# Kernel tuning notes

Hardware: AMD Instinct MI355X
Metric: run time of the kernel (lower is better)

The kernel has to match this reference:

```python
import jax, jax.numpy as jnp
import numpy as np

HIDDEN = 128
N_RBF = 20
K = 16
CUTOFF = 5.0


def setup_inputs() -> dict:
    key = jax.random.key(0)
    ks = jax.random.split(key, 12)
    B, N, D = 8, 4096, HIDDEN
    edge_in = 2 * D + N_RBF  # 276
    s = 0.02
    return {
        "h": jax.random.normal(ks[0], (B, N, D), jnp.float32),
        "positions": jax.random.normal(ks[1], (B, N, 3), jnp.float32),
        # edge MLP: Linear(276->128), SiLU, Linear(128->128), SiLU
        "ew1": jax.random.normal(ks[2], (edge_in, D), jnp.float32) * s,
        "eb1": jnp.zeros((D,), jnp.float32),
        "ew2": jax.random.normal(ks[3], (D, D), jnp.float32) * s,
        "eb2": jnp.zeros((D,), jnp.float32),
        # node MLP: Linear(256->128), SiLU, (Dropout=identity in eval), Linear(128->128)
        "nw1": jax.random.normal(ks[4], (2 * D, D), jnp.float32) * s,
        "nb1": jnp.zeros((D,), jnp.float32),
        "nw2": jax.random.normal(ks[5], (D, D), jnp.float32) * s,
        "nb2": jnp.zeros((D,), jnp.float32),
        # LayerNorm
        "gamma": jnp.ones((D,), jnp.float32),
        "beta": jnp.zeros((D,), jnp.float32),
    }


def reference(h, positions, ew1, eb1, ew2, eb2, nw1, nb1, nw2, nb2, gamma, beta):
    B, N, D = h.shape
    k = min(K, N - 1)

    # ---- kNN graph build (dense pairwise, self masked with +inf) ----
    diff = positions[:, :, None, :] - positions[:, None, :, :]      # [B,N,N,3]
    dists = jnp.sqrt(jnp.sum(diff * diff, axis=-1) + 1e-8)          # [B,N,N]
    eye = jnp.eye(N, dtype=bool)
    dists_masked = jnp.where(eye[None], jnp.inf, dists)
    _, edge_idx = jax.lax.top_k(-dists_masked, k)                   # [B,N,k] smallest dists
    edge_dist = jnp.take_along_axis(dists_masked, edge_idx, axis=-1)  # [B,N,k]
    edge_mask = edge_dist < CUTOFF                                  # [B,N,k]

    # ---- RBF distance encoding (non-trainable buffers) ----
    centers = jnp.linspace(0.0, CUTOFF, N_RBF)                      # [n_rbf]
    widths = (CUTOFF / N_RBF) ** (-2)
    rbf = jnp.exp(-widths * (edge_dist[..., None] - centers) ** 2)  # [B,N,k,n_rbf]

    # ---- gather neighbor features ----
    h_j = jax.vmap(lambda hb, ib: hb[ib])(h, edge_idx)              # [B,N,k,D]
    h_i = jnp.broadcast_to(h[:, :, None, :], h_j.shape)             # [B,N,k,D]
    edge_features = jnp.concatenate([h_i, h_j, rbf], axis=-1)       # [B,N,k,2D+n_rbf]

    # ---- edge MLP + mask + scatter-sum aggregate ----
    m = jax.nn.silu(edge_features @ ew1 + eb1)
    m = jax.nn.silu(m @ ew2 + eb2)
    m = m * edge_mask[..., None].astype(m.dtype)
    agg = jnp.sum(m, axis=2)                                        # [B,N,D]

    # ---- node MLP (dropout is identity at eval) + residual + LayerNorm ----
    node_in = jnp.concatenate([h, agg], axis=-1)                    # [B,N,2D]
    update = jax.nn.silu(node_in @ nw1 + nb1) @ nw2 + nb2
    x = h + update
    mu = jnp.mean(x, axis=-1, keepdims=True)
    var = jnp.mean((x - mu) ** 2, axis=-1, keepdims=True)
    return (x - mu) / jnp.sqrt(var + 1e-5) * gamma + beta
```

## Files before the change

kernel.cpp:

```cpp
#include <hip/hip_runtime.h>

#define HID 128
#define NRBF 20
#define KNN 16
#define NNODE 4096
#define NBATCH 8
#define CAP 112

typedef __attribute__((ext_vector_type(8))) short short8;
typedef __attribute__((ext_vector_type(4))) float f32x4;

__device__ __forceinline__ short f2bf(float x) {
  unsigned u = __builtin_bit_cast(unsigned, x);
  u = u + 0x7FFFu + ((u >> 16) & 1u);
  return (short)(u >> 16);
}
__device__ __forceinline__ float silu_f(float x) {
  return x * __builtin_amdgcn_rcpf(1.0f + __expf(-x));
}
__device__ __forceinline__ short8 cv8(const float* p) {
  f32x4 a = *(const f32x4*)p;
  f32x4 b = *(const f32x4*)(p + 4);
  short8 r;
  r[0]=f2bf(a[0]); r[1]=f2bf(a[1]); r[2]=f2bf(a[2]); r[3]=f2bf(a[3]);
  r[4]=f2bf(b[0]); r[5]=f2bf(b[1]); r[6]=f2bf(b[2]); r[7]=f2bf(b[3]);
  return r;
}

__global__ __launch_bounds__(256)
void hcvt_kernel(const float* __restrict__ h, short* __restrict__ hb)
{
  size_t i = ((size_t)blockIdx.x * 256 + threadIdx.x) * 8;
  *(short8*)(hb + i) = cv8(h + i);
}

__global__ __launch_bounds__(512)
void knn_kernel(const float* __restrict__ pos,
                int* __restrict__ eidx, float* __restrict__ edist)
{
  __shared__ float pX[NNODE], pY[NNODE], pZ[NNODE];
  __shared__ float d2b[8][4][CAP];
  __shared__ int   jb[8][4][CAP];
  __shared__ int   cntL[8][4];

  const int tid  = threadIdx.x;
  const int wv   = tid >> 6;
  const int lane = tid & 63;
  const int b    = blockIdx.x >> 7;
  const int grp  = blockIdx.x & 127;

  const float* pb = pos + (size_t)b * NNODE * 3;
  for (int idx = tid; idx < NNODE; idx += 512) {
    pX[idx] = pb[idx*3]; pY[idx] = pb[idx*3+1]; pZ[idx] = pb[idx*3+2];
  }
  __syncthreads();

  const int i0 = grp * 32 + wv * 4;
  float pix[4], piy[4], piz[4];
  #pragma unroll
  for (int n = 0; n < 4; ++n) { pix[n]=pX[i0+n]; piy[n]=pY[i0+n]; piz[n]=pZ[i0+n]; }

  float vmin0[4] = {3.0e38f, 3.0e38f, 3.0e38f, 3.0e38f};
  float vmin1[4] = {3.0e38f, 3.0e38f, 3.0e38f, 3.0e38f};
  #pragma unroll 4
  for (int t = 0; t < 64; t += 2) {
    const int j0 = t*64 + lane, j1 = j0 + 64;
    const float x0 = pX[j0], y0 = pY[j0], z0 = pZ[j0];
    const float x1 = pX[j1], y1 = pY[j1], z1 = pZ[j1];
    #pragma unroll
    for (int n = 0; n < 4; ++n) {
      float dx0 = pix[n]-x0, dy0 = piy[n]-y0, dz0 = piz[n]-z0;
      vmin0[n] = fminf(vmin0[n], fmaf(dz0,dz0, fmaf(dy0,dy0, dx0*dx0)));
      float dx1 = pix[n]-x1, dy1 = piy[n]-y1, dz1 = piz[n]-z1;
      vmin1[n] = fminf(vmin1[n], fmaf(dz1,dz1, fmaf(dy1,dy1, dx1*dx1)));
    }
  }

  float Tp[4];
  #pragma unroll
  for (int n = 0; n < 4; ++n) {
    float v = fminf(vmin0[n], vmin1[n]);
    #pragma unroll
    for (int k = 2; k <= 64; k <<= 1) {
      #pragma unroll
      for (int jj = k >> 1; jj > 0; jj >>= 1) {
        float o = __shfl_xor(v, jj);
        const bool up   = ((lane & k) == 0);
        const bool lowl = ((lane & jj) == 0);
        float mn = fminf(v, o), mx = fmaxf(v, o);
        v = (up == lowl) ? mn : mx;
      }
    }
    float Tf = __shfl(v, 16);
    Tp[n] = Tf * (1.0f + 2.0e-6f) + 1.0e-35f;
  }

  if (lane < 4) cntL[wv][lane] = 0;
  #pragma unroll 2
  for (int t = 0; t < 64; ++t) {
    const int j = t * 64 + lane;
    const float x = pX[j], y = pY[j], z = pZ[j];
    #pragma unroll
    for (int n = 0; n < 4; ++n) {
      float dx = pix[n] - x, dy = piy[n] - y, dz = piz[n] - z;
      float d2 = fmaf(dz, dz, fmaf(dy, dy, dx * dx));
      if ((j != i0 + n) && (d2 <= Tp[n])) {
        int p = atomicAdd(&cntL[wv][n], 1);
        if (p < CAP) jb[wv][n][p] = j;
      }
    }
  }

  #pragma unroll 1
  for (int n = 0; n < 4; ++n) {
    int cnt = cntL[wv][n];
    if (cnt > CAP) cnt = CAP;
    for (int s = lane; s < cnt; s += 64) {
      int j = jb[wv][n][s];
      float dx = __fsub_rn(pix[n], pX[j]);
      float dy = __fsub_rn(piy[n], pY[j]);
      float dz = __fsub_rn(piz[n], pZ[j]);
      d2b[wv][n][s] = __fadd_rn(__fadd_rn(__fmul_rn(dx,dx), __fmul_rn(dy,dy)),
                                __fmul_rn(dz,dz));
    }
    for (int s = lane; s < cnt; s += 64) {
      float dm = d2b[wv][n][s]; int jm = jb[wv][n][s];
      int rank = 0;
      for (int c = 0; c < cnt; ++c) {
        float dc = d2b[wv][n][c]; int jc = jb[wv][n][c];
        if (dc < dm || (dc == dm && jc < jm)) ++rank;
      }
      if (rank < KNN) {
        size_t base = ((size_t)b * NNODE + i0 + n) * KNN;
        eidx[base + rank]  = b * NNODE + jm;
        edist[base + rank] = sqrtf(__fadd_rn(dm, 1e-8f));
      }
    }
  }
}

#define ENPW 16

template<bool HBF>
__global__ __launch_bounds__(512)
void edge_kernel(const float* __restrict__ h, const short* __restrict__ hb,
                 const int* __restrict__ eidx, const float* __restrict__ edist,
                 const float* __restrict__ ew1, const float* __restrict__ eb1,
                 const float* __restrict__ ew2, const float* __restrict__ eb2,
                 float* __restrict__ agg)
{
  __shared__ __attribute__((aligned(16))) short8 F1[9*8*64];
  __shared__ __attribute__((aligned(16))) short8 F2[4*8*64];
  __shared__ __attribute__((aligned(16))) short m1s[8][2048];

  const int tid = threadIdx.x;
  for (int f = tid; f < 9*8*64; f += 512) {
    int kc = f >> 9, rem = f & 511, nf = rem >> 6, ln = rem & 63;
    int kb = kc*32 + (ln >> 4)*8, col = nf*16 + (ln & 15);
    short8 v;
    #pragma unroll
    for (int e = 0; e < 8; ++e) {
      int k = kb + e;
      v[e] = (k < 276) ? f2bf(ew1[k*128 + col]) : (short)0;
    }
    F1[f] = v;
  }
  for (int f = tid; f < 4*8*64; f += 512) {
    int kc = f >> 9, rem = f & 511, nf = rem >> 6, ln = rem & 63;
    int kb = kc*32 + (ln >> 4)*8, col = nf*16 + (ln & 15);
    short8 v;
    #pragma unroll
    for (int e = 0; e < 8; ++e) v[e] = f2bf(ew2[(kb + e)*128 + col]);
    F2[f] = v;
  }
  __syncthreads();

  const int wv = tid >> 6, lane = tid & 63;
  const int lo = lane & 15, hi = lane >> 4;
  short* m1w = &m1s[wv][0];

  float b1v[8], b2v[8];
  #pragma unroll
  for (int nf = 0; nf < 8; ++nf) {
    b1v[nf] = eb1[nf*16 + lo];
    b2v[nf] = eb2[nf*16 + lo];
  }
  int wbase[4], xmask[4], rbase[4];
  #pragma unroll
  for (int q = 0; q < 4; ++q) {
    int row = hi*4 + q;
    wbase[q] = (row << 8) + (lo << 1);
    xmask[q] = (row & 7) << 4;
  }
  #pragma unroll
  for (int kc = 0; kc < 4; ++kc)
    rbase[kc] = ((lo << 8) + ((kc*32 + hi*8) << 1)) ^ ((lo & 7) << 4);

  const f32x4 zero4 = {0.f, 0.f, 0.f, 0.f};
  const int swz = (blockIdx.x & 7) * 32 + (blockIdx.x >> 3);
  const int nbase = (swz * 8 + wv) * ENPW;

  #pragma unroll 1
  for (int it = 0; it < ENPW/2; ++it) {
    const int nA = nbase + it*2, nB = nA + 1;
    int jgA = eidx[(size_t)nA*KNN + lo] & (NBATCH*NNODE - 1);
    int jgB = eidx[(size_t)nB*KNN + lo] & (NBATCH*NNODE - 1);
    const float deA = edist[(size_t)nA*KNN + lo];
    const float deB = edist[(size_t)nB*KNN + lo];

    short8 aIA[4], aJA[4], aIB[4], aJB[4];
    #pragma unroll
    for (int kc = 0; kc < 4; ++kc) {
      if constexpr (HBF) {
        aIA[kc] = *(const short8*)(hb + (size_t)nA*HID  + kc*32 + hi*8);
        aJA[kc] = *(const short8*)(hb + (size_t)jgA*HID + kc*32 + hi*8);
        aIB[kc] = *(const short8*)(hb + (size_t)nB*HID  + kc*32 + hi*8);
        aJB[kc] = *(const short8*)(hb + (size_t)jgB*HID + kc*32 + hi*8);
      } else {
        aIA[kc] = cv8(h + (size_t)nA*HID  + kc*32 + hi*8);
        aJA[kc] = cv8(h + (size_t)jgA*HID + kc*32 + hi*8);
        aIB[kc] = cv8(h + (size_t)nB*HID  + kc*32 + hi*8);
        aJB[kc] = cv8(h + (size_t)jgB*HID + kc*32 + hi*8);
      }
    }
    short8 aRA, aRB;
    #pragma unroll
    for (int e = 0; e < 8; ++e) {
      const int r = hi*8 + e;
      float vA = 0.f, vB = 0.f;
      if (r < NRBF) {
        const float cr = (float)(r * (5.0/19.0));
        float tA = __fsub_rn(deA, cr), tB = __fsub_rn(deB, cr);
        vA = __expf(-16.0f * __fmul_rn(tA, tA));
        vB = __expf(-16.0f * __fmul_rn(tB, tB));
      }
      aRA[e] = f2bf(vA); aRB[e] = f2bf(vB);
    }

    f32x4 acc1A[8], acc1B[8];
    #pragma unroll
    for (int nf = 0; nf < 8; ++nf) { acc1A[nf] = zero4; acc1B[nf] = zero4; }
    __builtin_amdgcn_s_setprio(1);
    #pragma unroll
    for (int kc = 0; kc < 9; ++kc) {
      short8 aA = (kc < 4) ? aIA[kc] : ((kc < 8) ? aJA[kc-4] : aRA);
      short8 aB = (kc < 4) ? aIB[kc] : ((kc < 8) ? aJB[kc-4] : aRB);
      #pragma unroll
      for (int nf = 0; nf < 8; ++nf) {
        short8 bfv = F1[(kc*8 + nf)*64 + lane];
        acc1A[nf] = __builtin_amdgcn_mfma_f32_16x16x32_bf16(aA, bfv, acc1A[nf], 0,0,0);
        acc1B[nf] = __builtin_amdgcn_mfma_f32_16x16x32_bf16(aB, bfv, acc1B[nf], 0,0,0);
      }
    }
    __builtin_amdgcn_s_setprio(0);

    short8 a2A[4], a2B[4];
    #pragma unroll
    for (int nf = 0; nf < 8; ++nf) {
      #pragma unroll
      for (int q = 0; q < 4; ++q) {
        int off = (wbase[q] + (nf << 5)) ^ xmask[q];
        *(short*)((char*)m1w + off) = f2bf(silu_f(acc1A[nf][q] + b1v[nf]));
      }
    }
    #pragma unroll
    for (int kc = 0; kc < 4; ++kc)
      a2A[kc] = *(const short8*)((char*)m1w + rbase[kc]);
    #pragma unroll
    for (int nf = 0; nf < 8; ++nf) {
      #pragma unroll
      for (int q = 0; q < 4; ++q) {
        int off = (wbase[q] + (nf << 5)) ^ xmask[q];
        *(short*)((char*)m1w + off) = f2bf(silu_f(acc1B[nf][q] + b1v[nf]));
      }
    }
    #pragma unroll
    for (int kc = 0; kc < 4; ++kc)
      a2B[kc] = *(const short8*)((char*)m1w + rbase[kc]);

    f32x4 acc2A[8], acc2B[8];
    #pragma unroll
    for (int nf = 0; nf < 8; ++nf) { acc2A[nf] = zero4; acc2B[nf] = zero4; }
    __builtin_amdgcn_s_setprio(1);
    #pragma unroll
    for (int kc = 0; kc < 4; ++kc) {
      #pragma unroll
      for (int nf = 0; nf < 8; ++nf) {
        short8 bfv = F2[(kc*8 + nf)*64 + lane];
        acc2A[nf] = __builtin_amdgcn_mfma_f32_16x16x32_bf16(a2A[kc], bfv, acc2A[nf], 0,0,0);
        acc2B[nf] = __builtin_amdgcn_mfma_f32_16x16x32_bf16(a2B[kc], bfv, acc2B[nf], 0,0,0);
      }
    }
    __builtin_amdgcn_s_setprio(0);

    float dqA[4], dqB[4];
    #pragma unroll
    for (int q = 0; q < 4; ++q) {
      dqA[q] = __shfl(deA, hi*4 + q);
      dqB[q] = __shfl(deB, hi*4 + q);
    }
    #pragma unroll
    for (int nf = 0; nf < 8; ++nf) {
      float sA = 0.f, sB = 0.f;
      #pragma unroll
      for (int q = 0; q < 4; ++q) {
        float mA = silu_f(acc2A[nf][q] + b2v[nf]);
        float mB = silu_f(acc2B[nf][q] + b2v[nf]);
        sA += (dqA[q] < 5.0f) ? mA : 0.f;
        sB += (dqB[q] < 5.0f) ? mB : 0.f;
      }
      sA += __shfl_xor(sA, 16); sA += __shfl_xor(sA, 32);
      sB += __shfl_xor(sB, 16); sB += __shfl_xor(sB, 32);
      if (hi == 0) {
        agg[(size_t)nA*HID + nf*16 + lo] = sA;
        agg[(size_t)nB*HID + nf*16 + lo] = sB;
      }
    }
  }
}

template<bool HBF>
__global__ __launch_bounds__(512)
void node_kernel(const float* __restrict__ h, const short* __restrict__ hb,
                 const float* agg,
                 const float* __restrict__ nw1, const float* __restrict__ nb1,
                 const float* __restrict__ nw2, const float* __restrict__ nb2,
                 const float* __restrict__ gam, const float* __restrict__ bet,
                 float* out)
{
  __shared__ __attribute__((aligned(16))) short8 G1[8*8*64];
  __shared__ __attribute__((aligned(16))) short8 G2[4*8*64];
  __shared__ __attribute__((aligned(16))) short m1s[8][2048];

  const int tid = threadIdx.x;
  for (int f = tid; f < 8*8*64; f += 512) {
    int kc = f >> 9, rem = f & 511, nf = rem >> 6, ln = rem & 63;
    int kb = kc*32 + (ln >> 4)*8, col = nf*16 + (ln & 15);
    short8 v;
    #pragma unroll
    for (int e = 0; e < 8; ++e) v[e] = f2bf(nw1[(kb + e)*128 + col]);
    G1[f] = v;
  }
  for (int f = tid; f < 4*8*64; f += 512) {
    int kc = f >> 9, rem = f & 511, nf = rem >> 6, ln = rem & 63;
    int kb = kc*32 + (ln >> 4)*8, col = nf*16 + (ln & 15);
    short8 v;
    #pragma unroll
    for (int e = 0; e < 8; ++e) v[e] = f2bf(nw2[(kb + e)*128 + col]);
    G2[f] = v;
  }
  __syncthreads();

  const int wv = tid >> 6, lane = tid & 63;
  const int lo = lane & 15, hi = lane >> 4;
  short* m1w = &m1s[wv][0];

  float b1v[8], b2v[8], gv[8], bv[8];
  #pragma unroll
  for (int nf = 0; nf < 8; ++nf) {
    b1v[nf] = nb1[nf*16 + lo];
    b2v[nf] = nb2[nf*16 + lo];
    gv[nf]  = gam[nf*16 + lo];
    bv[nf]  = bet[nf*16 + lo];
  }
  const f32x4 zero4 = {0.f, 0.f, 0.f, 0.f};

  const int row0 = (blockIdx.x * 8 + wv) * 16;

  const float* hrow = h   + (size_t)(row0 + lo) * HID;
  const float* arow = agg + (size_t)(row0 + lo) * HID;
  const short* hbrow = hb + (size_t)(row0 + lo) * HID;

  f32x4 acc1[8];
  #pragma unroll
  for (int nf = 0; nf < 8; ++nf) acc1[nf] = zero4;
  #pragma unroll
  for (int kc = 0; kc < 8; ++kc) {
    short8 a;
    if (kc < 4) {
      if constexpr (HBF) a = *(const short8*)(hbrow + kc*32 + hi*8);
      else               a = cv8(hrow + kc*32 + hi*8);
    } else {
      a = cv8(arow + (kc - 4)*32 + hi*8);
    }
    #pragma unroll
    for (int nf = 0; nf < 8; ++nf) {
      short8 bfv = G1[(kc*8 + nf)*64 + lane];
      acc1[nf] = __builtin_amdgcn_mfma_f32_16x16x32_bf16(a, bfv, acc1[nf], 0,0,0);
    }
  }

  #pragma unroll
  for (int nf = 0; nf < 8; ++nf) {
    #pragma unroll
    for (int q = 0; q < 4; ++q) {
      float s = silu_f(acc1[nf][q] + b1v[nf]);
      int row = hi*4 + q, col = nf*16 + lo;
      int byteoff = ((row << 8) + (col << 1)) ^ ((row & 7) << 4);
      *(short*)((char*)m1w + byteoff) = f2bf(s);
    }
  }

  f32x4 acc2[8];
  #pragma unroll
  for (int nf = 0; nf < 8; ++nf) acc2[nf] = zero4;
  #pragma unroll
  for (int kc = 0; kc < 4; ++kc) {
    int byteA = ((lo << 8) + ((kc*32 + hi*8) << 1)) ^ ((lo & 7) << 4);
    short8 a = *(const short8*)((char*)m1w + byteA);
    #pragma unroll
    for (int nf = 0; nf < 8; ++nf) {
      short8 bfv = G2[(kc*8 + nf)*64 + lane];
      acc2[nf] = __builtin_amdgcn_mfma_f32_16x16x32_bf16(a, bfv, acc2[nf], 0,0,0);
    }
  }

  float xv[4][8];
  #pragma unroll
  for (int nf = 0; nf < 8; ++nf) {
    #pragma unroll
    for (int q = 0; q < 4; ++q) {
      xv[q][nf] = acc2[nf][q] + b2v[nf]
                + h[(size_t)(row0 + hi*4 + q) * HID + nf*16 + lo];
    }
  }

  #pragma unroll
  for (int q = 0; q < 4; ++q) {
    float s = 0.0f;
    #pragma unroll
    for (int nf = 0; nf < 8; ++nf) s += xv[q][nf];
    s += __shfl_xor(s, 1); s += __shfl_xor(s, 2);
    s += __shfl_xor(s, 4); s += __shfl_xor(s, 8);
    float mu = s * 0.0078125f;
    float t = 0.0f;
    #pragma unroll
    for (int nf = 0; nf < 8; ++nf) { float d = xv[q][nf] - mu; t += d * d; }
    t += __shfl_xor(t, 1); t += __shfl_xor(t, 2);
    t += __shfl_xor(t, 4); t += __shfl_xor(t, 8);
    float inv = 1.0f / sqrtf(t * 0.0078125f + 1e-5f);
    #pragma unroll
    for (int nf = 0; nf < 8; ++nf) {
      float y = (xv[q][nf] - mu) * inv * gv[nf] + bv[nf];
      out[(size_t)(row0 + hi*4 + q) * HID + nf*16 + lo] = y;
    }
  }
}

extern "C" void kernel_launch(void* const* d_in, const int* in_sizes, int n_in,
                              void* d_out, int out_size, void* d_ws, size_t ws_size,
                              hipStream_t stream) {
  (void)in_sizes; (void)n_in; (void)out_size;
  const float* h   = (const float*)d_in[0];
  const float* pos = (const float*)d_in[1];
  const float* ew1 = (const float*)d_in[2];
  const float* eb1 = (const float*)d_in[3];
  const float* ew2 = (const float*)d_in[4];
  const float* eb2 = (const float*)d_in[5];
  const float* nw1 = (const float*)d_in[6];
  const float* nb1 = (const float*)d_in[7];
  const float* nw2 = (const float*)d_in[8];
  const float* nb2 = (const float*)d_in[9];
  const float* gam = (const float*)d_in[10];
  const float* bet = (const float*)d_in[11];

  const size_t base_need = (size_t)NBATCH * NNODE * KNN * 8;
  const size_t hbf_need  = base_need + (size_t)NBATCH * NNODE * HID * 2;
  if (ws_size < base_need) return;
  const bool use_hbf = (ws_size >= hbf_need);

  char* wsp = (char*)d_ws;
  int*   eidx  = (int*)wsp;
  float* edist = (float*)(wsp + (size_t)NBATCH * NNODE * KNN * 4);
  short* hb    = (short*)(wsp + base_need);
  float* agg   = (float*)d_out;

  if (use_hbf) {
    hcvt_kernel<<<dim3(2048), dim3(256), 0, stream>>>(h, hb);
  }
  knn_kernel<<<dim3(1024), dim3(512), 0, stream>>>(pos, eidx, edist);
  if (use_hbf) {
    edge_kernel<true ><<<dim3(256), dim3(512), 0, stream>>>(h, hb, eidx, edist,
                                                            ew1, eb1, ew2, eb2, agg);
    node_kernel<true ><<<dim3(256), dim3(512), 0, stream>>>(h, hb, agg, nw1, nb1,
                                                            nw2, nb2, gam, bet, (float*)d_out);
  } else {
    edge_kernel<false><<<dim3(256), dim3(512), 0, stream>>>(h, hb, eidx, edist,
                                                            ew1, eb1, ew2, eb2, agg);
    node_kernel<false><<<dim3(256), dim3(512), 0, stream>>>(h, hb, agg, nw1, nb1,
                                                            nw2, nb2, gam, bet, (float*)d_out);
  }
}
```

Measured before the change: 204.1 us.

## Use packed fp16 kNN prefilter and split edge MLP into two kernels

The kNN kernel now stores positions in shared memory as packed half2 and runs the threshold and candidate-filter passes in fp16. The threshold is widened to absorb fp16 error, and exact distances are recomputed in fp32 from global memory. The fused edge kernel is split into edge1 and edge2 kernels that pass a bf16 hidden activation through a large workspace buffer. This aims to cut kNN ALU and LDS cost and raise edge-MLP occupancy, at the price of extra global traffic. A looser threshold can overflow the candidate capacity, and fp16 may misrank near-ties.

```diff
diff --git a/kernel.cpp b/kernel.cpp
--- a/kernel.cpp
+++ b/kernel.cpp
@@ -9,6 +9,7 @@
 
 typedef __attribute__((ext_vector_type(8))) short short8;
 typedef __attribute__((ext_vector_type(4))) float f32x4;
+typedef __attribute__((ext_vector_type(2))) _Float16 h2;
 
 __device__ __forceinline__ short f2bf(float x) {
   unsigned u = __builtin_bit_cast(unsigned, x);
@@ -38,7 +39,7 @@
 void knn_kernel(const float* __restrict__ pos,
                 int* __restrict__ eidx, float* __restrict__ edist)
 {
-  __shared__ float pX[NNODE], pY[NNODE], pZ[NNODE];
+  __shared__ h2 pHx[NNODE/2], pHy[NNODE/2], pHz[NNODE/2];
   __shared__ float d2b[8][4][CAP];
   __shared__ int   jb[8][4][CAP];
   __shared__ int   cntL[8][4];
@@ -50,36 +51,49 @@
   const int grp  = blockIdx.x & 127;
 
   const float* pb = pos + (size_t)b * NNODE * 3;
-  for (int idx = tid; idx < NNODE; idx += 512) {
-    pX[idx] = pb[idx*3]; pY[idx] = pb[idx*3+1]; pZ[idx] = pb[idx*3+2];
+  for (int k = tid; k < NNODE/2; k += 512) {
+    h2 vx, vy, vz;
+    vx[0] = (_Float16)pb[(2*k)*3];   vx[1] = (_Float16)pb[(2*k+1)*3];
+    vy[0] = (_Float16)pb[(2*k)*3+1]; vy[1] = (_Float16)pb[(2*k+1)*3+1];
+    vz[0] = (_Float16)pb[(2*k)*3+2]; vz[1] = (_Float16)pb[(2*k+1)*3+2];
+    pHx[k] = vx; pHy[k] = vy; pHz[k] = vz;
   }
   __syncthreads();
 
   const int i0 = grp * 32 + wv * 4;
-  float pix[4], piy[4], piz[4];
-  #pragma unroll
-  for (int n = 0; n < 4; ++n) { pix[n]=pX[i0+n]; piy[n]=pY[i0+n]; piz[n]=pZ[i0+n]; }
-
-  float vmin0[4] = {3.0e38f, 3.0e38f, 3.0e38f, 3.0e38f};
-  float vmin1[4] = {3.0e38f, 3.0e38f, 3.0e38f, 3.0e38f};
-  #pragma unroll 4
-  for (int t = 0; t < 64; t += 2) {
-    const int j0 = t*64 + lane, j1 = j0 + 64;
-    const float x0 = pX[j0], y0 = pY[j0], z0 = pZ[j0];
-    const float x1 = pX[j1], y1 = pY[j1], z1 = pZ[j1];
+  float pixf[4], piyf[4], pizf[4];
+  h2 px2[4], py2[4], pz2[4];
+  #pragma unroll
+  for (int n = 0; n < 4; ++n) {
+    pixf[n] = pb[(i0+n)*3]; piyf[n] = pb[(i0+n)*3+1]; pizf[n] = pb[(i0+n)*3+2];
+    _Float16 hx = (_Float16)pixf[n], hy = (_Float16)piyf[n], hz = (_Float16)pizf[n];
+    px2[n][0] = hx; px2[n][1] = hx;
+    py2[n][0] = hy; py2[n][1] = hy;
+    pz2[n][0] = hz; pz2[n][1] = hz;
+  }
+
+  h2 vmin2[4];
+  #pragma unroll
+  for (int n = 0; n < 4; ++n) { vmin2[n][0] = (_Float16)6.0e4f; vmin2[n][1] = (_Float16)6.0e4f; }
+  #pragma unroll 2
+  for (int t = 0; t < 32; ++t) {
+    const int k = t*64 + lane;
+    h2 xh = pHx[k], yh = pHy[k], zh = pHz[k];
     #pragma unroll
     for (int n = 0; n < 4; ++n) {
-      float dx0 = pix[n]-x0, dy0 = piy[n]-y0, dz0 = piz[n]-z0;
-      vmin0[n] = fminf(vmin0[n], fmaf(dz0,dz0, fmaf(dy0,dy0, dx0*dx0)));
-      float dx1 = pix[n]-x1, dy1 = piy[n]-y1, dz1 = piz[n]-z1;
-      vmin1[n] = fminf(vmin1[n], fmaf(dz1,dz1, fmaf(dy1,dy1, dx1*dx1)));
+      h2 dx = px2[n] - xh;
+      h2 dy = py2[n] - yh;
+      h2 dz = pz2[n] - zh;
+      h2 d2 = dz*dz + dy*dy + dx*dx;
+      vmin2[n] = __builtin_elementwise_min(vmin2[n], d2);
     }
   }
 
   float Tp[4];
+  _Float16 TpH[4];
   #pragma unroll
   for (int n = 0; n < 4; ++n) {
-    float v = fminf(vmin0[n], vmin1[n]);
+    float v = fminf((float)vmin2[n][0], (float)vmin2[n][1]);
     #pragma unroll
     for (int k = 2; k <= 64; k <<= 1) {
       #pragma unroll
@@ -92,21 +106,29 @@
       }
     }
     float Tf = __shfl(v, 16);
-    Tp[n] = Tf * (1.0f + 2.0e-6f) + 1.0e-35f;
+    Tp[n]  = Tf * 1.6f + 1.0e-3f;
+    TpH[n] = (_Float16)(Tp[n] * 1.01f);
   }
 
   if (lane < 4) cntL[wv][lane] = 0;
   #pragma unroll 2
-  for (int t = 0; t < 64; ++t) {
-    const int j = t * 64 + lane;
-    const float x = pX[j], y = pY[j], z = pZ[j];
+  for (int t = 0; t < 32; ++t) {
+    const int k = t*64 + lane;
+    h2 xh = pHx[k], yh = pHy[k], zh = pHz[k];
+    const int j0 = 2*k, j1 = 2*k + 1;
     #pragma unroll
     for (int n = 0; n < 4; ++n) {
-      float dx = pix[n] - x, dy = piy[n] - y, dz = piz[n] - z;
-      float d2 = fmaf(dz, dz, fmaf(dy, dy, dx * dx));
-      if ((j != i0 + n) && (d2 <= Tp[n])) {
+      h2 dx = px2[n] - xh;
+      h2 dy = py2[n] - yh;
+      h2 dz = pz2[n] - zh;
+      h2 d2 = dz*dz + dy*dy + dx*dx;
+      if ((d2[0] <= TpH[n]) && (j0 != i0 + n)) {
         int p = atomicAdd(&cntL[wv][n], 1);
-        if (p < CAP) jb[wv][n][p] = j;
+        if (p < CAP) jb[wv][n][p] = j0;
+      }
+      if ((d2[1] <= TpH[n]) && (j1 != i0 + n)) {
+        int p = atomicAdd(&cntL[wv][n], 1);
+        if (p < CAP) jb[wv][n][p] = j1;
       }
     }
   }
@@ -117,9 +139,9 @@
     if (cnt > CAP) cnt = CAP;
     for (int s = lane; s < cnt; s += 64) {
       int j = jb[wv][n][s];
-      float dx = __fsub_rn(pix[n], pX[j]);
-      float dy = __fsub_rn(piy[n], pY[j]);
-      float dz = __fsub_rn(piz[n], pZ[j]);
+      float dx = __fsub_rn(pixf[n], pb[j*3]);
+      float dy = __fsub_rn(piyf[n], pb[j*3+1]);
+      float dz = __fsub_rn(pizf[n], pb[j*3+2]);
       d2b[wv][n][s] = __fadd_rn(__fadd_rn(__fmul_rn(dx,dx), __fmul_rn(dy,dy)),
                                 __fmul_rn(dz,dz));
     }
@@ -134,6 +156,182 @@
         size_t base = ((size_t)b * NNODE + i0 + n) * KNN;
         eidx[base + rank]  = b * NNODE + jm;
         edist[base + rank] = sqrtf(__fadd_rn(dm, 1e-8f));
+      }
+    }
+  }
+}
+
+__global__ __launch_bounds__(512, 2)
+void edge1_kernel(const short* __restrict__ hb,
+                  const int* __restrict__ eidx, const float* __restrict__ edist,
+                  const float* __restrict__ ew1, const float* __restrict__ eb1,
+                  short* __restrict__ m1ws)
+{
+  __shared__ __attribute__((aligned(16))) short8 F1[9*8*64];
+
+  const int tid = threadIdx.x;
+  for (int f = tid; f < 9*8*64; f += 512) {
+    int kc = f >> 9, rem = f & 511, nf = rem >> 6, ln = rem & 63;
+    int kb = kc*32 + (ln >> 4)*8, col = nf*16 + (ln & 15);
+    short8 v;
+    #pragma unroll
+    for (int e = 0; e < 8; ++e) {
+      int k = kb + e;
+      v[e] = (k < 276) ? f2bf(ew1[k*128 + col]) : (short)0;
+    }
+    F1[f] = v;
+  }
+  __syncthreads();
+
+  const int wv = tid >> 6, lane = tid & 63;
+  const int lo = lane & 15, hi = lane >> 4;
+
+  float b1v[8];
+  #pragma unroll
+  for (int nf = 0; nf < 8; ++nf) b1v[nf] = eb1[nf*16 + lo];
+
+  const f32x4 zero4 = {0.f, 0.f, 0.f, 0.f};
+  const int swz = (blockIdx.x & 7) * 64 + (blockIdx.x >> 3);
+  const int pbase = (swz * 8 + wv) * 4;
+
+  #pragma unroll 1
+  for (int it = 0; it < 4; ++it) {
+    const int p = pbase + it;
+    const int nA = p*2, nB = nA + 1;
+    int jgA = eidx[(size_t)nA*KNN + lo] & (NBATCH*NNODE - 1);
+    int jgB = eidx[(size_t)nB*KNN + lo] & (NBATCH*NNODE - 1);
+    const float deA = edist[(size_t)nA*KNN + lo];
+    const float deB = edist[(size_t)nB*KNN + lo];
+
+    short8 aRA, aRB;
+    #pragma unroll
+    for (int e = 0; e < 8; ++e) {
+      const int r = hi*8 + e;
+      float vA = 0.f, vB = 0.f;
+      if (r < NRBF) {
+        const float cr = (float)(r * (5.0/19.0));
+        float tA = __fsub_rn(deA, cr), tB = __fsub_rn(deB, cr);
+        vA = __expf(-16.0f * __fmul_rn(tA, tA));
+        vB = __expf(-16.0f * __fmul_rn(tB, tB));
+      }
+      aRA[e] = f2bf(vA); aRB[e] = f2bf(vB);
+    }
+
+    f32x4 acc1A[8], acc1B[8];
+    #pragma unroll
+    for (int nf = 0; nf < 8; ++nf) { acc1A[nf] = zero4; acc1B[nf] = zero4; }
+    __builtin_amdgcn_s_setprio(1);
+    #pragma unroll
+    for (int kc = 0; kc < 9; ++kc) {
+      short8 aA, aB;
+      if (kc < 4) {
+        aA = *(const short8*)(hb + (size_t)nA*HID  + kc*32 + hi*8);
+        aB = *(const short8*)(hb + (size_t)nB*HID  + kc*32 + hi*8);
+      } else if (kc < 8) {
+        aA = *(const short8*)(hb + (size_t)jgA*HID + (kc-4)*32 + hi*8);
+        aB = *(const short8*)(hb + (size_t)jgB*HID + (kc-4)*32 + hi*8);
+      } else {
+        aA = aRA; aB = aRB;
+      }
+      #pragma unroll
+      for (int nf = 0; nf < 8; ++nf) {
+        short8 bfv = F1[(kc*8 + nf)*64 + lane];
+        acc1A[nf] = __builtin_amdgcn_mfma_f32_16x16x32_bf16(aA, bfv, acc1A[nf], 0,0,0);
+        acc1B[nf] = __builtin_amdgcn_mfma_f32_16x16x32_bf16(aB, bfv, acc1B[nf], 0,0,0);
+      }
+    }
+    __builtin_amdgcn_s_setprio(0);
+
+    short* mA = m1ws + (size_t)nA*2048 + hi*16 + lo;
+    short* mB = m1ws + (size_t)nB*2048 + hi*16 + lo;
+    #pragma unroll
+    for (int nf = 0; nf < 8; ++nf) {
+      #pragma unroll
+      for (int q = 0; q < 4; ++q) {
+        mA[(q*8 + nf)*64] = f2bf(silu_f(acc1A[nf][q] + b1v[nf]));
+        mB[(q*8 + nf)*64] = f2bf(silu_f(acc1B[nf][q] + b1v[nf]));
+      }
+    }
+  }
+}
+
+__global__ __launch_bounds__(512, 2)
+void edge2_kernel(const short* __restrict__ m1ws, const float* __restrict__ edist,
+                  const float* __restrict__ ew2, const float* __restrict__ eb2,
+                  float* __restrict__ agg)
+{
+  __shared__ __attribute__((aligned(16))) short8 F2[4*8*64];
+
+  const int tid = threadIdx.x;
+  for (int f = tid; f < 4*8*64; f += 512) {
+    int kc = f >> 9, rem = f & 511, nf = rem >> 6, ln = rem & 63;
+    int kb = kc*32 + (ln >> 4)*8, col = nf*16 + (ln & 15);
+    short8 v;
+    #pragma unroll
+    for (int e = 0; e < 8; ++e) v[e] = f2bf(ew2[(kb + e)*128 + col]);
+    F2[f] = v;
+  }
+  __syncthreads();
+
+  const int wv = tid >> 6, lane = tid & 63;
+  const int lo = lane & 15, hi = lane >> 4;
+
+  float b2v[8];
+  #pragma unroll
+  for (int nf = 0; nf < 8; ++nf) b2v[nf] = eb2[nf*16 + lo];
+
+  const int aoffbase = ((lo & 3)*8 + (hi >> 1))*64 + (lo >> 2)*16 + (hi & 1)*8;
+  const f32x4 zero4 = {0.f, 0.f, 0.f, 0.f};
+  const int pbase = (blockIdx.x * 8 + wv) * 4;
+
+  #pragma unroll 1
+  for (int it = 0; it < 4; ++it) {
+    const int p = pbase + it;
+    const int nA = p*2, nB = nA + 1;
+    const float deA = edist[(size_t)nA*KNN + lo];
+    const float deB = edist[(size_t)nB*KNN + lo];
+
+    const short* bA = m1ws + (size_t)nA*2048 + aoffbase;
+    const short* bB = m1ws + (size_t)nB*2048 + aoffbase;
+
+    f32x4 acc2A[8], acc2B[8];
+    #pragma unroll
+    for (int nf = 0; nf < 8; ++nf) { acc2A[nf] = zero4; acc2B[nf] = zero4; }
+    __builtin_amdgcn_s_setprio(1);
+    #pragma unroll
+    for (int kc = 0; kc < 4; ++kc) {
+      short8 aA = *(const short8*)(bA + kc*128);
+      short8 aB = *(const short8*)(bB + kc*128);
+      #pragma unroll
+      for (int nf = 0; nf < 8; ++nf) {
+        short8 bfv = F2[(kc*8 + nf)*64 + lane];
+        acc2A[nf] = __builtin_amdgcn_mfma_f32_16x16x32_bf16(aA, bfv, acc2A[nf], 0,0,0);
+        acc2B[nf] = __builtin_amdgcn_mfma_f32_16x16x32_bf16(aB, bfv, acc2B[nf], 0,0,0);
+      }
+    }
+    __builtin_amdgcn_s_setprio(0);
+
+    float dqA[4], dqB[4];
+    #pragma unroll
+    for (int q = 0; q < 4; ++q) {
+      dqA[q] = __shfl(deA, hi*4 + q);
+      dqB[q] = __shfl(deB, hi*4 + q);
+    }
+    #pragma unroll
+    for (int nf = 0; nf < 8; ++nf) {
+      float sA = 0.f, sB = 0.f;
+      #pragma unroll
+      for (int q = 0; q < 4; ++q) {
+        float mA = silu_f(acc2A[nf][q] + b2v[nf]);
+        float mB = silu_f(acc2B[nf][q] + b2v[nf]);
+        sA += (dqA[q] < 5.0f) ? mA : 0.f;
+        sB += (dqB[q] < 5.0f) ? mB : 0.f;
+      }
+      sA += __shfl_xor(sA, 16); sA += __shfl_xor(sA, 32);
+      sB += __shfl_xor(sB, 16); sB += __shfl_xor(sB, 32);
+      if (hi == 0) {
+        agg[(size_t)nA*HID + nf*16 + lo] = sA;
+        agg[(size_t)nB*HID + nf*16 + lo] = sB;
       }
     }
   }
@@ -464,29 +662,40 @@
   const float* gam = (const float*)d_in[10];
   const float* bet = (const float*)d_in[11];
 
-  const size_t base_need = (size_t)NBATCH * NNODE * KNN * 8;
-  const size_t hbf_need  = base_need + (size_t)NBATCH * NNODE * HID * 2;
-  if (ws_size < base_need) return;
-  const bool use_hbf = (ws_size >= hbf_need);
+  const size_t sz_ed = (size_t)NBATCH * NNODE * KNN * 8;
+  const size_t sz_hb = (size_t)NBATCH * NNODE * HID * 2;
+  const size_t sz_m1 = (size_t)NBATCH * NNODE * KNN * HID * 2;
+  if (ws_size < sz_ed) return;
+  const bool use_hbf   = (ws_size >= sz_ed + sz_hb);
+  const bool use_split = (ws_size >= sz_ed + sz_hb + sz_m1);
 
   char* wsp = (char*)d_ws;
   int*   eidx  = (int*)wsp;
-  float* edist = (float*)(wsp + (size_t)NBATCH * NNODE * KNN * 4);
-  short* hb    = (short*)(wsp + base_need);
+  float* edist = (float*)(wsp + sz_ed / 2);
+  short* hb    = (short*)(wsp + sz_ed);
+  short* m1ws  = (short*)(wsp + sz_ed + sz_hb);
   float* agg   = (float*)d_out;
 
   if (use_hbf) {
     hcvt_kernel<<<dim3(2048), dim3(256), 0, stream>>>(h, hb);
   }
   knn_kernel<<<dim3(1024), dim3(512), 0, stream>>>(pos, eidx, edist);
-  if (use_hbf) {
+
+  if (use_split) {
+    edge1_kernel<<<dim3(512), dim3(512), 0, stream>>>(hb, eidx, edist, ew1, eb1, m1ws);
+    edge2_kernel<<<dim3(512), dim3(512), 0, stream>>>(m1ws, edist, ew2, eb2, agg);
+  } else if (use_hbf) {
     edge_kernel<true ><<<dim3(256), dim3(512), 0, stream>>>(h, hb, eidx, edist,
                                                             ew1, eb1, ew2, eb2, agg);
+  } else {
+    edge_kernel<false><<<dim3(256), dim3(512), 0, stream>>>(h, hb, eidx, edist,
+                                                            ew1, eb1, ew2, eb2, agg);
+  }
+
+  if (use_hbf) {
     node_kernel<true ><<<dim3(256), dim3(512), 0, stream>>>(h, hb, agg, nw1, nb1,
                                                             nw2, nb2, gam, bet, (float*)d_out);
   } else {
-    edge_kernel<false><<<dim3(256), dim3(512), 0, stream>>>(h, hb, eidx, edist,
-                                                            ew1, eb1, ew2, eb2, agg);
     node_kernel<false><<<dim3(256), dim3(512), 0, stream>>>(h, hb, agg, nw1, nb1,
                                                             nw2, nb2, gam, bet, (float*)d_out);
   }
```

New measurement: 417.4 us. +104.5%, slower.
